# Performance work log

Hardware: AMD Instinct MI355X
Metric: run time of the kernel (lower is better)

The kernel has to match this reference:

```python
import jax, jax.numpy as jnp
import numpy as np
from jax import lax

B, S, D = 4, 2048, 256      # batch, seq_len, hidden_dim
F = 1024                    # ffn_dim
E = 32                      # num_experts
K = 4                       # top_k


def setup_inputs() -> dict:
    key = jax.random.key(0)
    ks = jax.random.split(key, 5)
    scale = 0.02
    x = jax.random.normal(ks[0], (B, S, D), dtype=jnp.float32)
    router_w = jax.random.normal(ks[1], (E, D), dtype=jnp.float32) * scale   # gate Linear weight [out=E, in=D]
    w_gate = jax.random.normal(ks[2], (E, F, D), dtype=jnp.float32) * scale  # per-expert [F, D]
    w_up = jax.random.normal(ks[3], (E, F, D), dtype=jnp.float32) * scale
    w_down = jax.random.normal(ks[4], (E, D, F), dtype=jnp.float32) * scale
    return {"x": x, "router_w": router_w, "w_gate": w_gate, "w_up": w_up, "w_down": w_down}


def reference(x, router_w, w_gate, w_up, w_down):
    # Eval mode: jitter noise and dropout are inactive (training-only in the source).
    b, s, d = x.shape
    T = b * s
    xf = x.reshape(T, d)                                   # [T, D]

    # --- Router ---
    logits = xf @ router_w.T                               # [T, E]
    tk_logits, tk_idx = lax.top_k(logits, K)               # [T, K]
    tk_w = jax.nn.softmax(tk_logits, axis=-1)              # [T, K]
    probs = jax.nn.softmax(logits, axis=-1)                # [T, E]
    one_hot = jax.nn.one_hot(tk_idx, E, dtype=x.dtype)     # [T, K, E]
    tokens_per_expert = one_hot.sum(axis=(0, 1))           # [E]
    f_frac = tokens_per_expert / T
    P = probs.mean(axis=0)
    aux_loss = E * (f_frac * P).sum()

    # combine[t, e] = sum_k tk_w[t,k] * [tk_idx[t,k] == e]
    combine = jnp.einsum("tk,tke->te", tk_w, one_hot)      # [T, E]

    # --- Experts: scan over experts, SwiGLU FFN, weighted accumulate ---
    def step(acc, params):
        wg, wu, wd, ce = params                            # [F,D], [F,D], [D,F], [T]
        h = jax.nn.silu(xf @ wg.T) * (xf @ wu.T)           # [T, F]
        return acc + ce[:, None] * (h @ wd.T), None

    out, _ = lax.scan(step, jnp.zeros_like(xf),
                      (w_gate, w_up, w_down, combine.T))
    return out.reshape(b, s, d), aux_loss
```

## Files before the change

### kernel.cpp

```cpp
#include <hip/hip_runtime.h>
#include <math.h>

#define TOK 8192
#define DIM 256
#define NE  32
#define NK  4
#define NF  1024

typedef __bf16 bf16x8 __attribute__((ext_vector_type(8)));
typedef float  f32x4  __attribute__((ext_vector_type(4)));
typedef unsigned short u16x8 __attribute__((ext_vector_type(8)));

__device__ __forceinline__ unsigned short f2b(float f) {
  unsigned u = __builtin_bit_cast(unsigned, f);
  unsigned r = (u + 0x7FFFu + ((u >> 16) & 1u)) >> 16;
  return (unsigned short)r;
}

__device__ __forceinline__ void gload16(const void* g, void* l) {
  __builtin_amdgcn_global_load_lds(
      (const __attribute__((address_space(1))) void*)g,
      (__attribute__((address_space(3))) void*)l, 16, 0, 0);
}

__global__ __launch_bounds__(256) void router_kernel(
    const float* __restrict__ x, const float* __restrict__ rw,
    int* __restrict__ counts, float* __restrict__ psum,
    int* __restrict__ etok, float* __restrict__ ewt,
    float* __restrict__ outz)
{
  __shared__ float xs[32][DIM + 4];
  __shared__ float ws[NE][DIM + 4];
  __shared__ float lg[32][NE];
  __shared__ int hist[NE];
  __shared__ int base[NE];

  const int tid = threadIdx.x;
  const int t0 = blockIdx.x * 32;

  {
    float4 z4 = {0.f, 0.f, 0.f, 0.f};
    float4* og = (float4*)(outz + (size_t)t0 * DIM);
    #pragma unroll
    for (int i = 0; i < 8; i++) og[i*256 + tid] = z4;
  }

  {
    const float4* xg = (const float4*)(x + (size_t)t0 * DIM);
    for (int i = tid; i < 32 * (DIM/4); i += 256) {
      int t = i / (DIM/4), c = i % (DIM/4);
      *(float4*)&xs[t][c*4] = xg[t*(DIM/4)+c];
    }
    const float4* wgp = (const float4*)rw;
    for (int i = tid; i < NE * (DIM/4); i += 256) {
      int e = i / (DIM/4), c = i % (DIM/4);
      *(float4*)&ws[e][c*4] = wgp[e*(DIM/4)+c];
    }
  }
  if (tid < NE) hist[tid] = 0;
  __syncthreads();

  for (int i = 0; i < 4; i++) {
    int idx = i*256 + tid;
    int t = idx >> 5, e = idx & 31;
    float acc = 0.f;
    for (int c = 0; c < DIM/4; c++) {
      float4 a = *(const float4*)&xs[t][c*4];
      float4 b = *(const float4*)&ws[e][c*4];
      acc += a.x*b.x + a.y*b.y + a.z*b.z + a.w*b.w;
    }
    lg[t][e] = acc;
  }
  __syncthreads();

  int ids[NK]; int slots[NK]; float wts[NK];
  if (tid < 32) {
    const int t = tid;
    float l[NE];
    #pragma unroll
    for (int e = 0; e < NE; e++) l[e] = lg[t][e];
    unsigned mask = 0;
    float vals[NK];
    #pragma unroll
    for (int k = 0; k < NK; k++) {
      float best = -INFINITY; int bi = 0;
      for (int e = 0; e < NE; e++)
        if (!((mask >> e) & 1u) && l[e] > best) { best = l[e]; bi = e; }
      mask |= 1u << bi; vals[k] = best; ids[k] = bi;
    }
    float s4 = 0.f;
    #pragma unroll
    for (int k = 0; k < NK; k++) { wts[k] = __expf(vals[k] - vals[0]); s4 += wts[k]; }
    #pragma unroll
    for (int k = 0; k < NK; k++) wts[k] /= s4;
    float s = 0.f;
    for (int e = 0; e < NE; e++) { l[e] = __expf(l[e] - vals[0]); s += l[e]; }
    float inv = 1.f / s;
    for (int e = 0; e < NE; e++) lg[t][e] = l[e] * inv;
    #pragma unroll
    for (int k = 0; k < NK; k++) slots[k] = atomicAdd(&hist[ids[k]], 1);
  }
  __syncthreads();
  if (tid < NE) {
    float s = 0.f;
    for (int t = 0; t < 32; t++) s += lg[t][tid];
    atomicAdd(&psum[tid], s);
    int h = hist[tid];
    base[tid] = h ? atomicAdd(&counts[tid], h) : 0;
  }
  __syncthreads();
  if (tid < 32) {
    #pragma unroll
    for (int k = 0; k < NK; k++) {
      int p = base[ids[k]] + slots[k];
      etok[(size_t)ids[k]*TOK + p] = t0 + tid;
      ewt [(size_t)ids[k]*TOK + p] = wts[k];
    }
  }
}

__global__ void aux_kernel(const int* __restrict__ counts,
                           const float* __restrict__ psum,
                           float* __restrict__ aux_out)
{
  int tid = threadIdx.x;
  float v = 0.f;
  if (tid < NE) v = (counts[tid] / (float)TOK) * (psum[tid] / (float)TOK);
  #pragma unroll
  for (int off = 32; off; off >>= 1) v += __shfl_down(v, off);
  if (tid == 0) aux_out[0] = (float)NE * v;
}

__global__ __launch_bounds__(256) void convert_kernel(
    const float* __restrict__ wg_, const float* __restrict__ wu_,
    const float* __restrict__ wd_, unsigned short* __restrict__ wB)
{
  int gid = blockIdx.x * 256 + threadIdx.x;
  int sg  = gid >> 11;
  int idx = gid & 2047;
  int e   = sg / 48;
  int st  = sg - e * 48;
  int ch  = st / 3;
  int ty  = st - ch * 3;
  unsigned short* dst = wB + ((size_t)sg << 14);
  const float* src;
  int pos;
  if (ty < 2) {
    int f = idx >> 5, gk = idx & 31;
    const float* w = (ty == 0) ? wg_ : wu_;
    src = w + (size_t)e * (NF*DIM) + (size_t)(ch*64 + f) * DIM + (gk << 3);
    pos = f*256 + ((gk ^ (f & 7)) << 3);
  } else {
    int d = idx >> 3, fg = idx & 7;
    src = wd_ + (size_t)e * (DIM*NF) + (size_t)d * NF + (ch << 6) + (fg << 3);
    pos = (d << 6) + ((fg ^ (d & 7)) << 3);
  }
  float4 a = *(const float4*)src;
  float4 c = *(const float4*)(src + 4);
  u16x8 v;
  v[0]=f2b(a.x); v[1]=f2b(a.y); v[2]=f2b(a.z); v[3]=f2b(a.w);
  v[4]=f2b(c.x); v[5]=f2b(c.y); v[6]=f2b(c.z); v[7]=f2b(c.w);
  *(u16x8*)&dst[pos] = v;
}

#define PWB(N) asm volatile("s_waitcnt vmcnt(" #N ") lgkmcnt(0)\n\ts_barrier" ::: "memory")

#define ISSUE_L(sl_) do {                                               \
    const unsigned short* sp_ = wE + ((size_t)(3*c0 + (sl_)) << 14);    \
    unsigned short* dp_ = &ring[(sl_) & 3][0];                          \
    _Pragma("unroll")                                                   \
    for (int i_ = 0; i_ < 4; i_++) {                                    \
      int o_ = (i_*512 + tid) << 3;                                     \
      gload16(sp_ + o_, dp_ + o_);                                      \
    }                                                                   \
  } while (0)

#define WI(sl_) do { const int ah_ = S - (sl_);                         \
    if (ah_ > 3)       { PWB(8); ISSUE_L((sl_) + 3); }                  \
    else if (ah_ == 3) { PWB(8); }                                      \
    else if (ah_ == 2) { PWB(4); }                                      \
    else               { PWB(0); } } while (0)

#define COMP_G(rs)                                                      \
  _Pragma("unroll")                                                     \
  for (int nt = 0; nt < 2; nt++) {                                      \
    const int fl = nw*32 + nt*16 + ln;                                  \
    const int rowb = fl*256, xo = fl & 7;                               \
    ga[nt][0] = (f32x4){0,0,0,0}; ga[nt][1] = (f32x4){0,0,0,0};         \
    _Pragma("unroll")                                                   \
    for (int kk = 0; kk < 8; kk++) {                                    \
      bf16x8 bg = *(const bf16x8*)&rs[rowb + (((kk*4 + q) ^ xo) << 3)]; \
      ga[nt][0] = __builtin_amdgcn_mfma_f32_16x16x32_bf16(xf[0][kk], bg, ga[nt][0], 0,0,0); \
      ga[nt][1] = __builtin_amdgcn_mfma_f32_16x16x32_bf16(xf[1][kk], bg, ga[nt][1], 0,0,0); \
    }                                                                   \
  }

#define COMP_U(rs)                                                      \
  _Pragma("unroll")                                                     \
  for (int nt = 0; nt < 2; nt++) {                                      \
    const int fl = nw*32 + nt*16 + ln;                                  \
    const int rowb = fl*256, xo = fl & 7;                               \
    f32x4 ua0 = (f32x4){0,0,0,0}, ua1 = (f32x4){0,0,0,0};               \
    _Pragma("unroll")                                                   \
    for (int kk = 0; kk < 8; kk++) {                                    \
      bf16x8 bu = *(const bf16x8*)&rs[rowb + (((kk*4 + q) ^ xo) << 3)]; \
      ua0 = __builtin_amdgcn_mfma_f32_16x16x32_bf16(xf[0][kk], bu, ua0, 0,0,0); \
      ua1 = __builtin_amdgcn_mfma_f32_16x16x32_bf16(xf[1][kk], bu, ua1, 0,0,0); \
    }                                                                   \
    _Pragma("unroll")                                                   \
    for (int rr = 0; rr < 4; rr++) {                                    \
      float g0 = ga[nt][0][rr], g1 = ga[nt][1][rr];                     \
      hs[mw*32      + q*4 + rr][fl] = f2b((g0 / (1.f + __expf(-g0))) * ua0[rr]); \
      hs[mw*32 + 16 + q*4 + rr][fl] = f2b((g1 / (1.f + __expf(-g1))) * ua1[rr]); \
    }                                                                   \
  }

#define COMP_D(rs)                                                      \
  _Pragma("unroll")                                                     \
  for (int kk = 0; kk < 2; kk++) {                                      \
    bf16x8 a0 = *(const bf16x8*)&hs[mw*32      + ln][kk*32 + q*8];      \
    bf16x8 a1 = *(const bf16x8*)&hs[mw*32 + 16 + ln][kk*32 + q*8];      \
    _Pragma("unroll")                                                   \
    for (int nt = 0; nt < 8; nt++) {                                    \
      const int d = nw*128 + nt*16 + ln;                                \
      bf16x8 bd = *(const bf16x8*)&rs[d*64 + (((kk*4 + q) ^ (d & 7)) << 3)]; \
      oacc[nt][0] = __builtin_amdgcn_mfma_f32_16x16x32_bf16(a0, bd, oacc[nt][0], 0,0,0); \
      oacc[nt][1] = __builtin_amdgcn_mfma_f32_16x16x32_bf16(a1, bd, oacc[nt][1], 0,0,0); \
    }                                                                   \
  }

__global__ __launch_bounds__(512, 2) void expert_mfma7_kernel(
    const float* __restrict__ x,
    const unsigned short* __restrict__ wB,
    const int* __restrict__ counts,
    const int* __restrict__ etok, const float* __restrict__ ewt,
    float* __restrict__ out)
{
  __shared__ unsigned short ring[4][16384];
  __shared__ unsigned short hs[128][72];
  __shared__ int   lel[128];
  __shared__ float lwt[128];
  __shared__ int   pfx[NE + 1];

  const int tid  = threadIdx.x;
  const int lane = tid & 63;
  const int wv   = tid >> 6;
  const int mw   = wv & 3;
  const int nw   = wv >> 2;
  const int q    = lane >> 4;
  const int ln   = lane & 15;

  if (tid == 0) {
    int acc = 0;
    #pragma unroll 1
    for (int e = 0; e < NE; e++) { pfx[e] = acc; acc += (counts[e] + 127) >> 7; }
    pfx[NE] = acc;
  }
  __syncthreads();

  const int U  = __builtin_amdgcn_readfirstlane(pfx[NE] << 4);
  const int ub = ((blockIdx.x & 7) << 5) | (blockIdx.x >> 3);
  int       u  = (ub * U) >> 8;
  const int u1 = ((ub + 1) * U) >> 8;

  #pragma unroll 1
  while (u < u1) {
    const int g = u >> 4;
    int ev = 0;
    #pragma unroll 1
    while (pfx[ev + 1] <= g) ev++;
    const int e   = __builtin_amdgcn_readfirstlane(ev);
    const int t   = __builtin_amdgcn_readfirstlane(g - pfx[e]);
    const int c0  = u & 15;
    const int c1  = (16 < c0 + (u1 - u)) ? 16 : (c0 + (u1 - u));
    const int cnt = __builtin_amdgcn_readfirstlane(counts[e]);
    const int t0  = t << 7;
    const unsigned short* wE = wB + (size_t)e * 48 * 16384;
    const int*   el = etok + (size_t)e * TOK;
    const float* ew = ewt  + (size_t)e * TOK;

    if (tid < 128) {
      int gt = t0 + tid;
      lel[tid] = (gt < cnt) ? el[gt] : -1;
      lwt[tid] = (gt < cnt) ? ew[gt] : 0.f;
    }
    __syncthreads();

    bf16x8 xf[2][8];
    #pragma unroll
    for (int m = 0; m < 2; m++) {
      int row = mw*32 + m*16 + ln;
      int tok = lel[row]; if (tok < 0) tok = 0;
      const float* xr = x + (size_t)tok * DIM;
      #pragma unroll
      for (int k = 0; k < 8; k++) {
        float4 a = *(const float4*)(xr + k*32 + q*8);
        float4 c = *(const float4*)(xr + k*32 + q*8 + 4);
        union { bf16x8 v; unsigned short s[8]; } tt;
        tt.s[0]=f2b(a.x); tt.s[1]=f2b(a.y); tt.s[2]=f2b(a.z); tt.s[3]=f2b(a.w);
        tt.s[4]=f2b(c.x); tt.s[5]=f2b(c.y); tt.s[6]=f2b(c.z); tt.s[7]=f2b(c.w);
        xf[m][k] = tt.v;
      }
    }

    f32x4 oacc[8][2];
    #pragma unroll
    for (int nt = 0; nt < 8; nt++) { oacc[nt][0] = (f32x4){0,0,0,0}; oacc[nt][1] = (f32x4){0,0,0,0}; }

    const int S = 3 * (c1 - c0);

    asm volatile("s_waitcnt vmcnt(0)" ::: "memory");
    ISSUE_L(0); ISSUE_L(1); ISSUE_L(2);

    f32x4 ga[2][2];

    #pragma unroll 1
    for (int c = c0; c < c1; c++) {
      const int sb = 3 * (c - c0);
      WI(sb    ); { const unsigned short* rs = ring[ sb      & 3]; COMP_G(rs); }
      WI(sb + 1); { const unsigned short* rs = ring[(sb + 1) & 3]; COMP_U(rs); }
      WI(sb + 2); { const unsigned short* rs = ring[(sb + 2) & 3]; COMP_D(rs); }
    }

    #pragma unroll
    for (int nt = 0; nt < 8; nt++) {
      int d = nw*128 + nt*16 + ln;
      #pragma unroll
      for (int m = 0; m < 2; m++)
        #pragma unroll
        for (int rr = 0; rr < 4; rr++) {
          int tl = mw*32 + m*16 + q*4 + rr;
          int tok = lel[tl];
          if (tok >= 0)
            atomicAdd(&out[(size_t)tok*DIM + d], lwt[tl] * oacc[nt][m][rr]);
        }
    }
    __syncthreads();

    u += c1 - c0;
  }
}

__global__ __launch_bounds__(512, 2) void expert_mfma5_kernel(
    const float* __restrict__ x,
    const float* __restrict__ wg_, const float* __restrict__ wu_,
    const float* __restrict__ wd_,
    const int* __restrict__ counts,
    const int* __restrict__ etok, const float* __restrict__ ewt,
    float* __restrict__ out)
{
  const int b  = blockIdx.x;
  const int j  = b >> 3;
  const int e  = (b & 7) + 8 * (j & 3);
  const int s0 = j >> 2;
  const int cnt = counts[e];

  __shared__ unsigned short stg[2][16384];
  __shared__ unsigned short hs[128][72];
  __shared__ int   lel[128];
  __shared__ float lwt[128];

  const int tid  = threadIdx.x;
  const int lane = tid & 63;
  const int wv   = tid >> 6;
  const int mw   = wv & 3;
  const int nw   = wv >> 2;
  const int q    = lane >> 4;
  const int ln   = lane & 15;

  int guOff[4], dOff[4], dRow[4], dFg[4];
  #pragma unroll
  for (int i = 0; i < 4; i++) {
    int G = i*512 + tid;
    int f = G >> 5, gk = G & 31;
    guOff[i] = f*256 + ((gk ^ (f & 7)) << 3);
    int d = G >> 3, fg = G & 7;
    dOff[i] = d*64 + ((fg ^ (d & 7)) << 3);
    dRow[i] = d; dFg[i] = fg;
  }

  const float* wgE = wg_ + (size_t)e * NF * DIM;
  const float* wuE = wu_ + (size_t)e * NF * DIM;
  const float* wdE = wd_ + (size_t)e * DIM * NF;

  const int*   el = etok + (size_t)e * TOK;
  const float* ew = ewt  + (size_t)e * TOK;

  for (int t0 = s0 * 128; t0 < cnt; t0 += 1024) {
    if (tid < 128) {
      int gt = t0 + tid;
      lel[tid] = (gt < cnt) ? el[gt] : -1;
      lwt[tid] = (gt < cnt) ? ew[gt] : 0.f;
    }
    __syncthreads();

    bf16x8 xf[2][8];
    #pragma unroll
    for (int m = 0; m < 2; m++) {
      int row = mw*32 + m*16 + ln;
      int tok = lel[row]; if (tok < 0) tok = 0;
      const float* xr = x + (size_t)tok * DIM;
      #pragma unroll
      for (int k = 0; k < 8; k++) {
        float4 a = *(const float4*)(xr + k*32 + q*8);
        float4 c = *(const float4*)(xr + k*32 + q*8 + 4);
        union { bf16x8 v; unsigned short s[8]; } t;
        t.s[0]=f2b(a.x); t.s[1]=f2b(a.y); t.s[2]=f2b(a.z); t.s[3]=f2b(a.w);
        t.s[4]=f2b(c.x); t.s[5]=f2b(c.y); t.s[6]=f2b(c.z); t.s[7]=f2b(c.w);
        xf[m][k] = t.v;
      }
    }

    f32x4 oacc[8][2];
    #pragma unroll
    for (int nt = 0; nt < 8; nt++) { oacc[nt][0] = (f32x4){0,0,0,0}; oacc[nt][1] = (f32x4){0,0,0,0}; }

    unsigned short* pA = stg[0];
    unsigned short* pB = stg[1];
    float4 r[8];

    {
      const float4* s4 = (const float4*)wgE;
      #pragma unroll
      for (int i = 0; i < 4; i++) { int G = i*512 + tid; r[2*i] = s4[2*G]; r[2*i+1] = s4[2*G+1]; }
      #pragma unroll
      for (int i = 0; i < 4; i++) {
        u16x8 v;
        v[0]=f2b(r[2*i].x);   v[1]=f2b(r[2*i].y);   v[2]=f2b(r[2*i].z);   v[3]=f2b(r[2*i].w);
        v[4]=f2b(r[2*i+1].x); v[5]=f2b(r[2*i+1].y); v[6]=f2b(r[2*i+1].z); v[7]=f2b(r[2*i+1].w);
        *(u16x8*)&pA[guOff[i]] = v;
      }
    }
    __syncthreads();

    f32x4 ga[2][2];

    for (int ch = 0; ch < 16; ch++) {
      {
        const float4* s4 = (const float4*)(wuE + (size_t)ch*16384);
        #pragma unroll
        for (int i = 0; i < 4; i++) { int G = i*512 + tid; r[2*i] = s4[2*G]; r[2*i+1] = s4[2*G+1]; }
      }
      #pragma unroll
      for (int nt = 0; nt < 2; nt++) {
        int fl = nw*32 + nt*16 + ln;
        int rowb = fl*256, xo = fl & 7;
        ga[nt][0] = (f32x4){0,0,0,0}; ga[nt][1] = (f32x4){0,0,0,0};
        #pragma unroll
        for (int kk = 0; kk < 8; kk++) {
          bf16x8 bg = *(const bf16x8*)&pA[rowb + (((kk*4 + q) ^ xo) << 3)];
          ga[nt][0] = __builtin_amdgcn_mfma_f32_16x16x32_bf16(xf[0][kk], bg, ga[nt][0], 0,0,0);
          ga[nt][1] = __builtin_amdgcn_mfma_f32_16x16x32_bf16(xf[1][kk], bg, ga[nt][1], 0,0,0);
        }
      }
      #pragma unroll
      for (int i = 0; i < 4; i++) {
        u16x8 v;
        v[0]=f2b(r[2*i].x);   v[1]=f2b(r[2*i].y);   v[2]=f2b(r[2*i].z);   v[3]=f2b(r[2*i].w);
        v[4]=f2b(r[2*i+1].x); v[5]=f2b(r[2*i+1].y); v[6]=f2b(r[2*i+1].z); v[7]=f2b(r[2*i+1].w);
        *(u16x8*)&pB[guOff[i]] = v;
      }
      __syncthreads();
      { unsigned short* t = pA; pA = pB; pB = t; }

      {
        #pragma unroll
        for (int i = 0; i < 4; i++) {
          const float4* p = (const float4*)(wdE + (size_t)dRow[i]*NF + ch*64 + dFg[i]*8);
          r[2*i] = p[0]; r[2*i+1] = p[1];
        }
      }
      #pragma unroll
      for (int nt = 0; nt < 2; nt++) {
        int fl = nw*32 + nt*16 + ln;
        int rowb = fl*256, xo = fl & 7;
        f32x4 ua0 = (f32x4){0,0,0,0}, ua1 = (f32x4){0,0,0,0};
        #pragma unroll
        for (int kk = 0; kk < 8; kk++) {
          bf16x8 bu = *(const bf16x8*)&pA[rowb + (((kk*4 + q) ^ xo) << 3)];
          ua0 = __builtin_amdgcn_mfma_f32_16x16x32_bf16(xf[0][kk], bu, ua0, 0,0,0);
          ua1 = __builtin_amdgcn_mfma_f32_16x16x32_bf16(xf[1][kk], bu, ua1, 0,0,0);
        }
        #pragma unroll
        for (int rr = 0; rr < 4; rr++) {
          float g0 = ga[nt][0][rr], g1 = ga[nt][1][rr];
          hs[mw*32      + q*4 + rr][fl] = f2b((g0 / (1.f + __expf(-g0))) * ua0[rr]);
          hs[mw*32 + 16 + q*4 + rr][fl] = f2b((g1 / (1.f + __expf(-g1))) * ua1[rr]);
        }
      }
      #pragma unroll
      for (int i = 0; i < 4; i++) {
        u16x8 v;
        v[0]=f2b(r[2*i].x);   v[1]=f2b(r[2*i].y);   v[2]=f2b(r[2*i].z);   v[3]=f2b(r[2*i].w);
        v[4]=f2b(r[2*i+1].x); v[5]=f2b(r[2*i+1].y); v[6]=f2b(r[2*i+1].z); v[7]=f2b(r[2*i+1].w);
        *(u16x8*)&pB[dOff[i]] = v;
      }
      __syncthreads();
      { unsigned short* t = pA; pA = pB; pB = t; }

      if (ch < 15) {
        const float4* s4 = (const float4*)(wgE + (size_t)(ch+1)*16384);
        #pragma unroll
        for (int i = 0; i < 4; i++) { int G = i*512 + tid; r[2*i] = s4[2*G]; r[2*i+1] = s4[2*G+1]; }
      }
      #pragma unroll
      for (int kk = 0; kk < 2; kk++) {
        bf16x8 a0 = *(const bf16x8*)&hs[mw*32      + ln][kk*32 + q*8];
        bf16x8 a1 = *(const bf16x8*)&hs[mw*32 + 16 + ln][kk*32 + q*8];
        #pragma unroll
        for (int nt = 0; nt < 8; nt++) {
          int d = nw*128 + nt*16 + ln;
          bf16x8 bd = *(const bf16x8*)&pA[d*64 + (((kk*4 + q) ^ (d & 7)) << 3)];
          oacc[nt][0] = __builtin_amdgcn_mfma_f32_16x16x32_bf16(a0, bd, oacc[nt][0], 0,0,0);
          oacc[nt][1] = __builtin_amdgcn_mfma_f32_16x16x32_bf16(a1, bd, oacc[nt][1], 0,0,0);
        }
      }
      if (ch < 15) {
        #pragma unroll
        for (int i = 0; i < 4; i++) {
          u16x8 v;
          v[0]=f2b(r[2*i].x);   v[1]=f2b(r[2*i].y);   v[2]=f2b(r[2*i].z);   v[3]=f2b(r[2*i].w);
          v[4]=f2b(r[2*i+1].x); v[5]=f2b(r[2*i+1].y); v[6]=f2b(r[2*i+1].z); v[7]=f2b(r[2*i+1].w);
          *(u16x8*)&pB[guOff[i]] = v;
        }
      }
      __syncthreads();
      { unsigned short* t = pA; pA = pB; pB = t; }
    }

    #pragma unroll
    for (int nt = 0; nt < 8; nt++) {
      int d = nw*128 + nt*16 + ln;
      #pragma unroll
      for (int m = 0; m < 2; m++)
        #pragma unroll
        for (int rr = 0; rr < 4; rr++) {
          int tl = mw*32 + m*16 + q*4 + rr;
          int tok = lel[tl];
          if (tok >= 0)
            atomicAdd(&out[(size_t)tok*DIM + d], lwt[tl] * oacc[nt][m][rr]);
        }
    }
    __syncthreads();
  }
}

extern "C" void kernel_launch(void* const* d_in, const int* in_sizes, int n_in,
                              void* d_out, int out_size, void* d_ws, size_t ws_size,
                              hipStream_t stream)
{
  const float* x  = (const float*)d_in[0];
  const float* rw = (const float*)d_in[1];
  const float* wg = (const float*)d_in[2];
  const float* wu = (const float*)d_in[3];
  const float* wd = (const float*)d_in[4];
  float* out = (float*)d_out;

  int*   counts = (int*)d_ws;
  float* psum   = (float*)((char*)d_ws + 128);
  int*   etok   = (int*)((char*)d_ws + 256);
  float* ewt    = (float*)((char*)d_ws + 256 + (size_t)NE*TOK*4);

  hipMemsetAsync(d_ws, 0, 256, stream);

  router_kernel<<<TOK/32, 256, 0, stream>>>(x, rw, counts, psum, etok, ewt, out);
  aux_kernel<<<1, 64, 0, stream>>>(counts, psum, out + (size_t)TOK*DIM);

  const size_t wboff = (size_t)4 << 20;
  const size_t wbsz  = (size_t)NE * 48 * 16384 * 2;
  if (ws_size >= wboff + wbsz) {
    unsigned short* wB = (unsigned short*)((char*)d_ws + wboff);
    convert_kernel<<<(NE*48*2048)/256, 256, 0, stream>>>(wg, wu, wd, wB);
    expert_mfma7_kernel<<<256, 512, 0, stream>>>(x, wB, counts, etok, ewt, out);
  } else {
    expert_mfma5_kernel<<<256, 512, 0, stream>>>(x, wg, wu, wd, counts, etok, ewt, out);
  }
}
```

Measured before the change: 317.5 us.

## Fuse router with weight conversion and retile expert waves to 2x4 layout

The router and the fp32-to-bf16 weight conversion now run in one launch: the first 256 blocks do routing and the remaining 1536 blocks each convert eight chunks of weights. This removes a kernel launch and lets the two independent stages overlap. The expert kernel's wave layout changes from 4 M-waves by 2 N-waves to 2 by 4, so each wave holds 64 token rows against 16 F columns (and 64 D columns in the down projection). Each B fragment read from LDS is then reused across four MFMAs instead of two, at the cost of more registers for the x fragments and accumulators.

After: 369.5 us. +16.4%, slower.

```diff
diff --git a/kernel.cpp b/kernel.cpp
--- a/kernel.cpp
+++ b/kernel.cpp
@@ -23,8 +23,8 @@
       (__attribute__((address_space(3))) void*)l, 16, 0, 0);
 }
 
-__global__ __launch_bounds__(256) void router_kernel(
-    const float* __restrict__ x, const float* __restrict__ rw,
+__device__ __forceinline__ void router_body(
+    int bid, const float* __restrict__ x, const float* __restrict__ rw,
     int* __restrict__ counts, float* __restrict__ psum,
     int* __restrict__ etok, float* __restrict__ ewt,
     float* __restrict__ outz)
@@ -36,7 +36,7 @@
   __shared__ int base[NE];
 
   const int tid = threadIdx.x;
-  const int t0 = blockIdx.x * 32;
+  const int t0 = bid * 32;
 
   {
     float4 z4 = {0.f, 0.f, 0.f, 0.f};
@@ -119,23 +119,10 @@
   }
 }
 
-__global__ void aux_kernel(const int* __restrict__ counts,
-                           const float* __restrict__ psum,
-                           float* __restrict__ aux_out)
-{
-  int tid = threadIdx.x;
-  float v = 0.f;
-  if (tid < NE) v = (counts[tid] / (float)TOK) * (psum[tid] / (float)TOK);
-  #pragma unroll
-  for (int off = 32; off; off >>= 1) v += __shfl_down(v, off);
-  if (tid == 0) aux_out[0] = (float)NE * v;
-}
-
-__global__ __launch_bounds__(256) void convert_kernel(
-    const float* __restrict__ wg_, const float* __restrict__ wu_,
+__device__ __forceinline__ void convert_body(
+    int gid, const float* __restrict__ wg_, const float* __restrict__ wu_,
     const float* __restrict__ wd_, unsigned short* __restrict__ wB)
 {
-  int gid = blockIdx.x * 256 + threadIdx.x;
   int sg  = gid >> 11;
   int idx = gid & 2047;
   int e   = sg / 48;
@@ -163,6 +150,45 @@
   *(u16x8*)&dst[pos] = v;
 }
 
+__global__ __launch_bounds__(256) void fused_rc_kernel(
+    const float* __restrict__ x, const float* __restrict__ rw,
+    const float* __restrict__ wg_, const float* __restrict__ wu_,
+    const float* __restrict__ wd_,
+    int* __restrict__ counts, float* __restrict__ psum,
+    int* __restrict__ etok, float* __restrict__ ewt,
+    float* __restrict__ outz, unsigned short* __restrict__ wB)
+{
+  if (blockIdx.x < 256) {
+    router_body(blockIdx.x, x, rw, counts, psum, etok, ewt, outz);
+  } else {
+    int gid = (blockIdx.x - 256) * 256 + threadIdx.x;
+    #pragma unroll
+    for (int it = 0; it < 8; it++, gid += 1536*256)
+      convert_body(gid, wg_, wu_, wd_, wB);
+  }
+}
+
+__global__ __launch_bounds__(256) void router_kernel(
+    const float* __restrict__ x, const float* __restrict__ rw,
+    int* __restrict__ counts, float* __restrict__ psum,
+    int* __restrict__ etok, float* __restrict__ ewt,
+    float* __restrict__ outz)
+{
+  router_body(blockIdx.x, x, rw, counts, psum, etok, ewt, outz);
+}
+
+__global__ void aux_kernel(const int* __restrict__ counts,
+                           const float* __restrict__ psum,
+                           float* __restrict__ aux_out)
+{
+  int tid = threadIdx.x;
+  float v = 0.f;
+  if (tid < NE) v = (counts[tid] / (float)TOK) * (psum[tid] / (float)TOK);
+  #pragma unroll
+  for (int off = 32; off; off >>= 1) v += __shfl_down(v, off);
+  if (tid == 0) aux_out[0] = (float)NE * v;
+}
+
 #define PWB(N) asm volatile("s_waitcnt vmcnt(" #N ") lgkmcnt(0)\n\ts_barrier" ::: "memory")
 
 #define ISSUE_L(sl_) do {                                               \
@@ -182,54 +208,56 @@
     else               { PWB(0); } } while (0)
 
 #define COMP_G(rs)                                                      \
-  _Pragma("unroll")                                                     \
-  for (int nt = 0; nt < 2; nt++) {                                      \
-    const int fl = nw*32 + nt*16 + ln;                                  \
+  { const int fl = nw*16 + ln;                                          \
     const int rowb = fl*256, xo = fl & 7;                               \
-    ga[nt][0] = (f32x4){0,0,0,0}; ga[nt][1] = (f32x4){0,0,0,0};         \
+    _Pragma("unroll")                                                   \
+    for (int m = 0; m < 4; m++) ga[m] = (f32x4){0,0,0,0};               \
     _Pragma("unroll")                                                   \
     for (int kk = 0; kk < 8; kk++) {                                    \
       bf16x8 bg = *(const bf16x8*)&rs[rowb + (((kk*4 + q) ^ xo) << 3)]; \
-      ga[nt][0] = __builtin_amdgcn_mfma_f32_16x16x32_bf16(xf[0][kk], bg, ga[nt][0], 0,0,0); \
-      ga[nt][1] = __builtin_amdgcn_mfma_f32_16x16x32_bf16(xf[1][kk], bg, ga[nt][1], 0,0,0); \
-    }                                                                   \
-  }
+      _Pragma("unroll")                                                 \
+      for (int m = 0; m < 4; m++)                                       \
+        ga[m] = __builtin_amdgcn_mfma_f32_16x16x32_bf16(xf[m][kk], bg, ga[m], 0,0,0); \
+    } }
 
 #define COMP_U(rs)                                                      \
-  _Pragma("unroll")                                                     \
-  for (int nt = 0; nt < 2; nt++) {                                      \
-    const int fl = nw*32 + nt*16 + ln;                                  \
+  { const int fl = nw*16 + ln;                                          \
     const int rowb = fl*256, xo = fl & 7;                               \
-    f32x4 ua0 = (f32x4){0,0,0,0}, ua1 = (f32x4){0,0,0,0};               \
+    f32x4 ua[4];                                                        \
+    _Pragma("unroll")                                                   \
+    for (int m = 0; m < 4; m++) ua[m] = (f32x4){0,0,0,0};               \
     _Pragma("unroll")                                                   \
     for (int kk = 0; kk < 8; kk++) {                                    \
       bf16x8 bu = *(const bf16x8*)&rs[rowb + (((kk*4 + q) ^ xo) << 3)]; \
-      ua0 = __builtin_amdgcn_mfma_f32_16x16x32_bf16(xf[0][kk], bu, ua0, 0,0,0); \
-      ua1 = __builtin_amdgcn_mfma_f32_16x16x32_bf16(xf[1][kk], bu, ua1, 0,0,0); \
+      _Pragma("unroll")                                                 \
+      for (int m = 0; m < 4; m++)                                       \
+        ua[m] = __builtin_amdgcn_mfma_f32_16x16x32_bf16(xf[m][kk], bu, ua[m], 0,0,0); \
     }                                                                   \
     _Pragma("unroll")                                                   \
-    for (int rr = 0; rr < 4; rr++) {                                    \
-      float g0 = ga[nt][0][rr], g1 = ga[nt][1][rr];                     \
-      hs[mw*32      + q*4 + rr][fl] = f2b((g0 / (1.f + __expf(-g0))) * ua0[rr]); \
-      hs[mw*32 + 16 + q*4 + rr][fl] = f2b((g1 / (1.f + __expf(-g1))) * ua1[rr]); \
-    }                                                                   \
-  }
+    for (int m = 0; m < 4; m++)                                         \
+      _Pragma("unroll")                                                 \
+      for (int rr = 0; rr < 4; rr++) {                                  \
+        float g0 = ga[m][rr];                                           \
+        hs[mw*64 + m*16 + q*4 + rr][fl] = f2b((g0 / (1.f + __expf(-g0))) * ua[m][rr]); \
+      } }
 
 #define COMP_D(rs)                                                      \
   _Pragma("unroll")                                                     \
   for (int kk = 0; kk < 2; kk++) {                                      \
-    bf16x8 a0 = *(const bf16x8*)&hs[mw*32      + ln][kk*32 + q*8];      \
-    bf16x8 a1 = *(const bf16x8*)&hs[mw*32 + 16 + ln][kk*32 + q*8];      \
-    _Pragma("unroll")                                                   \
-    for (int nt = 0; nt < 8; nt++) {                                    \
-      const int d = nw*128 + nt*16 + ln;                                \
+    bf16x8 a[4];                                                        \
+    _Pragma("unroll")                                                   \
+    for (int m = 0; m < 4; m++)                                         \
+      a[m] = *(const bf16x8*)&hs[mw*64 + m*16 + ln][kk*32 + q*8];       \
+    _Pragma("unroll")                                                   \
+    for (int nt = 0; nt < 4; nt++) {                                    \
+      const int d = nw*64 + nt*16 + ln;                                 \
       bf16x8 bd = *(const bf16x8*)&rs[d*64 + (((kk*4 + q) ^ (d & 7)) << 3)]; \
-      oacc[nt][0] = __builtin_amdgcn_mfma_f32_16x16x32_bf16(a0, bd, oacc[nt][0], 0,0,0); \
-      oacc[nt][1] = __builtin_amdgcn_mfma_f32_16x16x32_bf16(a1, bd, oacc[nt][1], 0,0,0); \
-    }                                                                   \
-  }
-
-__global__ __launch_bounds__(512, 2) void expert_mfma7_kernel(
+      _Pragma("unroll")                                                 \
+      for (int m = 0; m < 4; m++)                                       \
+        oacc[nt][m] = __builtin_amdgcn_mfma_f32_16x16x32_bf16(a[m], bd, oacc[nt][m], 0,0,0); \
+    } }
+
+__global__ __launch_bounds__(512, 2) void expert_mfma8_kernel(
     const float* __restrict__ x,
     const unsigned short* __restrict__ wB,
     const int* __restrict__ counts,
@@ -245,8 +273,8 @@
   const int tid  = threadIdx.x;
   const int lane = tid & 63;
   const int wv   = tid >> 6;
-  const int mw   = wv & 3;
-  const int nw   = wv >> 2;
+  const int mw   = wv & 1;
+  const int nw   = wv >> 1;
   const int q    = lane >> 4;
   const int ln   = lane & 15;
 
@@ -286,10 +314,10 @@
     }
     __syncthreads();
 
-    bf16x8 xf[2][8];
-    #pragma unroll
-    for (int m = 0; m < 2; m++) {
-      int row = mw*32 + m*16 + ln;
+    bf16x8 xf[4][8];
+    #pragma unroll
+    for (int m = 0; m < 4; m++) {
+      int row = mw*64 + m*16 + ln;
       int tok = lel[row]; if (tok < 0) tok = 0;
       const float* xr = x + (size_t)tok * DIM;
       #pragma unroll
@@ -303,16 +331,18 @@
       }
     }
 
-    f32x4 oacc[8][2];
-    #pragma unroll
-    for (int nt = 0; nt < 8; nt++) { oacc[nt][0] = (f32x4){0,0,0,0}; oacc[nt][1] = (f32x4){0,0,0,0}; }
+    f32x4 oacc[4][4];
+    #pragma unroll
+    for (int nt = 0; nt < 4; nt++)
+      #pragma unroll
+      for (int m = 0; m < 4; m++) oacc[nt][m] = (f32x4){0,0,0,0};
 
     const int S = 3 * (c1 - c0);
 
     asm volatile("s_waitcnt vmcnt(0)" ::: "memory");
     ISSUE_L(0); ISSUE_L(1); ISSUE_L(2);
 
-    f32x4 ga[2][2];
+    f32x4 ga[4];
 
     #pragma unroll 1
     for (int c = c0; c < c1; c++) {
@@ -323,13 +353,13 @@
     }
 
     #pragma unroll
-    for (int nt = 0; nt < 8; nt++) {
-      int d = nw*128 + nt*16 + ln;
-      #pragma unroll
-      for (int m = 0; m < 2; m++)
+    for (int nt = 0; nt < 4; nt++) {
+      int d = nw*64 + nt*16 + ln;
+      #pragma unroll
+      for (int m = 0; m < 4; m++)
         #pragma unroll
         for (int rr = 0; rr < 4; rr++) {
-          int tl = mw*32 + m*16 + q*4 + rr;
+          int tl = mw*64 + m*16 + q*4 + rr;
           int tok = lel[tl];
           if (tok >= 0)
             atomicAdd(&out[(size_t)tok*DIM + d], lwt[tl] * oacc[nt][m][rr]);
@@ -563,16 +593,17 @@
 
   hipMemsetAsync(d_ws, 0, 256, stream);
 
-  router_kernel<<<TOK/32, 256, 0, stream>>>(x, rw, counts, psum, etok, ewt, out);
-  aux_kernel<<<1, 64, 0, stream>>>(counts, psum, out + (size_t)TOK*DIM);
-
   const size_t wboff = (size_t)4 << 20;
   const size_t wbsz  = (size_t)NE * 48 * 16384 * 2;
   if (ws_size >= wboff + wbsz) {
     unsigned short* wB = (unsigned short*)((char*)d_ws + wboff);
-    convert_kernel<<<(NE*48*2048)/256, 256, 0, stream>>>(wg, wu, wd, wB);
-    expert_mfma7_kernel<<<256, 512, 0, stream>>>(x, wB, counts, etok, ewt, out);
+    fused_rc_kernel<<<256 + 1536, 256, 0, stream>>>(
+        x, rw, wg, wu, wd, counts, psum, etok, ewt, out, wB);
+    aux_kernel<<<1, 64, 0, stream>>>(counts, psum, out + (size_t)TOK*DIM);
+    expert_mfma8_kernel<<<256, 512, 0, stream>>>(x, wB, counts, etok, ewt, out);
   } else {
+    router_kernel<<<TOK/32, 256, 0, stream>>>(x, rw, counts, psum, etok, ewt, out);
+    aux_kernel<<<1, 64, 0, stream>>>(counts, psum, out + (size_t)TOK*DIM);
     expert_mfma5_kernel<<<256, 512, 0, stream>>>(x, wg, wu, wd, counts, etok, ewt, out);
   }
 }
```

## Fuse router and weight conversion into one launch; restructure expert prefetch schedule

Applied to the files above, without the earlier changes.

Router and bf16 weight-conversion kernels are merged into one launch: the first 256 blocks do routing and the remaining 1536 blocks each convert 8 chunks. This removes a launch gap and lets the two independent jobs overlap. Inside the expert kernel, the per-slot wait/issue sequence becomes a per-chunk schedule that waits twice per chunk and issues the next gate slice early, then two slices at once before the down projection. That means fewer barriers per chunk, at the cost of possibly shallower prefetch lookahead for some slices.

After: 325.0 us. 2.3% more time.

```diff
diff --git a/kernel.cpp b/kernel.cpp
--- a/kernel.cpp
+++ b/kernel.cpp
@@ -23,8 +23,8 @@
       (__attribute__((address_space(3))) void*)l, 16, 0, 0);
 }
 
-__global__ __launch_bounds__(256) void router_kernel(
-    const float* __restrict__ x, const float* __restrict__ rw,
+__device__ __forceinline__ void router_body(
+    int bid, const float* __restrict__ x, const float* __restrict__ rw,
     int* __restrict__ counts, float* __restrict__ psum,
     int* __restrict__ etok, float* __restrict__ ewt,
     float* __restrict__ outz)
@@ -36,7 +36,7 @@
   __shared__ int base[NE];
 
   const int tid = threadIdx.x;
-  const int t0 = blockIdx.x * 32;
+  const int t0 = bid * 32;
 
   {
     float4 z4 = {0.f, 0.f, 0.f, 0.f};
@@ -119,23 +119,10 @@
   }
 }
 
-__global__ void aux_kernel(const int* __restrict__ counts,
-                           const float* __restrict__ psum,
-                           float* __restrict__ aux_out)
-{
-  int tid = threadIdx.x;
-  float v = 0.f;
-  if (tid < NE) v = (counts[tid] / (float)TOK) * (psum[tid] / (float)TOK);
-  #pragma unroll
-  for (int off = 32; off; off >>= 1) v += __shfl_down(v, off);
-  if (tid == 0) aux_out[0] = (float)NE * v;
-}
-
-__global__ __launch_bounds__(256) void convert_kernel(
-    const float* __restrict__ wg_, const float* __restrict__ wu_,
+__device__ __forceinline__ void convert_body(
+    int gid, const float* __restrict__ wg_, const float* __restrict__ wu_,
     const float* __restrict__ wd_, unsigned short* __restrict__ wB)
 {
-  int gid = blockIdx.x * 256 + threadIdx.x;
   int sg  = gid >> 11;
   int idx = gid & 2047;
   int e   = sg / 48;
@@ -163,6 +150,45 @@
   *(u16x8*)&dst[pos] = v;
 }
 
+__global__ __launch_bounds__(256) void fused_rc_kernel(
+    const float* __restrict__ x, const float* __restrict__ rw,
+    const float* __restrict__ wg_, const float* __restrict__ wu_,
+    const float* __restrict__ wd_,
+    int* __restrict__ counts, float* __restrict__ psum,
+    int* __restrict__ etok, float* __restrict__ ewt,
+    float* __restrict__ outz, unsigned short* __restrict__ wB)
+{
+  if (blockIdx.x < 256) {
+    router_body(blockIdx.x, x, rw, counts, psum, etok, ewt, outz);
+  } else {
+    int gid = (blockIdx.x - 256) * 256 + threadIdx.x;
+    #pragma unroll
+    for (int it = 0; it < 8; it++, gid += 1536*256)
+      convert_body(gid, wg_, wu_, wd_, wB);
+  }
+}
+
+__global__ __launch_bounds__(256) void router_kernel(
+    const float* __restrict__ x, const float* __restrict__ rw,
+    int* __restrict__ counts, float* __restrict__ psum,
+    int* __restrict__ etok, float* __restrict__ ewt,
+    float* __restrict__ outz)
+{
+  router_body(blockIdx.x, x, rw, counts, psum, etok, ewt, outz);
+}
+
+__global__ void aux_kernel(const int* __restrict__ counts,
+                           const float* __restrict__ psum,
+                           float* __restrict__ aux_out)
+{
+  int tid = threadIdx.x;
+  float v = 0.f;
+  if (tid < NE) v = (counts[tid] / (float)TOK) * (psum[tid] / (float)TOK);
+  #pragma unroll
+  for (int off = 32; off; off >>= 1) v += __shfl_down(v, off);
+  if (tid == 0) aux_out[0] = (float)NE * v;
+}
+
 #define PWB(N) asm volatile("s_waitcnt vmcnt(" #N ") lgkmcnt(0)\n\ts_barrier" ::: "memory")
 
 #define ISSUE_L(sl_) do {                                               \
@@ -174,12 +200,6 @@
       gload16(sp_ + o_, dp_ + o_);                                      \
     }                                                                   \
   } while (0)
-
-#define WI(sl_) do { const int ah_ = S - (sl_);                         \
-    if (ah_ > 3)       { PWB(8); ISSUE_L((sl_) + 3); }                  \
-    else if (ah_ == 3) { PWB(8); }                                      \
-    else if (ah_ == 2) { PWB(4); }                                      \
-    else               { PWB(0); } } while (0)
 
 #define COMP_G(rs)                                                      \
   _Pragma("unroll")                                                     \
@@ -229,7 +249,7 @@
     }                                                                   \
   }
 
-__global__ __launch_bounds__(512, 2) void expert_mfma7_kernel(
+__global__ __launch_bounds__(512, 2) void expert_mfma9_kernel(
     const float* __restrict__ x,
     const unsigned short* __restrict__ wB,
     const int* __restrict__ counts,
@@ -317,9 +337,18 @@
     #pragma unroll 1
     for (int c = c0; c < c1; c++) {
       const int sb = 3 * (c - c0);
-      WI(sb    ); { const unsigned short* rs = ring[ sb      & 3]; COMP_G(rs); }
-      WI(sb + 1); { const unsigned short* rs = ring[(sb + 1) & 3]; COMP_U(rs); }
-      WI(sb + 2); { const unsigned short* rs = ring[(sb + 2) & 3]; COMP_D(rs); }
+      PWB(4);
+      if (sb + 3 < S) ISSUE_L(sb + 3);
+      { const unsigned short* rs = ring[ sb      & 3]; COMP_G(rs); }
+      { const unsigned short* rs = ring[(sb + 1) & 3]; COMP_U(rs); }
+      if (sb + 3 < S) {
+        PWB(4);
+        ISSUE_L(sb + 4);
+        ISSUE_L(sb + 5);
+      } else {
+        PWB(0);
+      }
+      { const unsigned short* rs = ring[(sb + 2) & 3]; COMP_D(rs); }
     }
 
     #pragma unroll
@@ -563,16 +592,17 @@
 
   hipMemsetAsync(d_ws, 0, 256, stream);
 
-  router_kernel<<<TOK/32, 256, 0, stream>>>(x, rw, counts, psum, etok, ewt, out);
-  aux_kernel<<<1, 64, 0, stream>>>(counts, psum, out + (size_t)TOK*DIM);
-
   const size_t wboff = (size_t)4 << 20;
   const size_t wbsz  = (size_t)NE * 48 * 16384 * 2;
   if (ws_size >= wboff + wbsz) {
     unsigned short* wB = (unsigned short*)((char*)d_ws + wboff);
-    convert_kernel<<<(NE*48*2048)/256, 256, 0, stream>>>(wg, wu, wd, wB);
-    expert_mfma7_kernel<<<256, 512, 0, stream>>>(x, wB, counts, etok, ewt, out);
+    fused_rc_kernel<<<256 + 1536, 256, 0, stream>>>(
+        x, rw, wg, wu, wd, counts, psum, etok, ewt, out, wB);
+    aux_kernel<<<1, 64, 0, stream>>>(counts, psum, out + (size_t)TOK*DIM);
+    expert_mfma9_kernel<<<256, 512, 0, stream>>>(x, wB, counts, etok, ewt, out);
   } else {
+    router_kernel<<<TOK/32, 256, 0, stream>>>(x, rw, counts, psum, etok, ewt, out);
+    aux_kernel<<<1, 64, 0, stream>>>(counts, psum, out + (size_t)TOK*DIM);
     expert_mfma5_kernel<<<256, 512, 0, stream>>>(x, wg, wu, wd, counts, etok, ewt, out);
   }
 }
```
